# Kernel tuning notes

Measured on AMD Instinct MI355X. Metric: run time of the kernel, lower is better.

Reference implementation:

```python
import jax, jax.numpy as jnp
from jax import lax
import numpy as np

# Bit order convention: pulse index 0 = MSB (sign bit), index 31 = LSB of mantissa.
SHIFTS = jnp.arange(31, -1, -1, dtype=jnp.uint32)  # [32]


def f32_to_pulses(x):
    """float32 [...] -> pulse bits [..., 32] in {0.,1.}"""
    u = lax.bitcast_convert_type(x.astype(jnp.float32), jnp.uint32)
    return ((u[..., None] >> SHIFTS) & jnp.uint32(1)).astype(jnp.float32)


def pulses_to_f32(p):
    """pulse bits [..., 32] -> float32 [...]"""
    bits = (p > 0.5).astype(jnp.uint32)
    u = jnp.sum(bits << SHIFTS, axis=-1).astype(jnp.uint32)
    return lax.bitcast_convert_type(u, jnp.float32)


def setup_inputs() -> dict:
    key = jax.random.key(0)
    kx, kw = jax.random.split(key)
    B, IN, OUT = 256, 1024, 1024
    x_f = jax.random.normal(kx, (B, IN), dtype=jnp.float32)
    w_f = jax.random.normal(kw, (OUT, IN), dtype=jnp.float32) * (1.0 / np.sqrt(IN))
    return {"x": f32_to_pulses(x_f), "weight_pulse": f32_to_pulses(w_f)}


def reference(x, weight_pulse):
    # Decode pulses to IEEE-754 FP32 values (exact: the spiking multiplier/adder
    # implement bit-exact FP32 arithmetic).
    xf = pulses_to_f32(x)              # [B, in]
    wf = pulses_to_f32(weight_pulse)   # [out, in]
    prods = xf[..., None, :] * wf      # [B, out, in]
    # SequentialAccumulator: strictly left-to-right FP32 accumulation (bit-exact
    # deterministic order), expressed as a scan over the in_features axis.
    acc0 = jnp.zeros(prods.shape[:-1], dtype=jnp.float32)  # [B, out]
    acc, _ = lax.scan(lambda a, p: (a + p, None), acc0, jnp.moveaxis(prods, -1, 0))
    # Re-encode the FP32 result to output pulses [B, out, 32].
    return f32_to_pulses(acc)
```

## Files before the change

### kernel.cpp

```cpp
#include <hip/hip_runtime.h>
#include <cstdint>

#define BATCH 256
#define INF   1024
#define OUTF  1024

__device__ __forceinline__ uint32_t assemble_bits(const float4* __restrict__ p4) {
    uint32_t u = 0;
#pragma unroll
    for (int j = 0; j < 8; ++j) {
        float4 v = p4[j];
        int sh = 31 - j * 4;
        u |= (v.x > 0.5f ? 1u : 0u) << sh;
        u |= (v.y > 0.5f ? 1u : 0u) << (sh - 1);
        u |= (v.z > 0.5f ? 1u : 0u) << (sh - 2);
        u |= (v.w > 0.5f ? 1u : 0u) << (sh - 3);
    }
    return u;
}

__global__ __launch_bounds__(256) void decode_pulses(
    const float* __restrict__ pulses, float* __restrict__ out, int n) {
    int i = blockIdx.x * blockDim.x + threadIdx.x;
    if (i >= n) return;
    const float4* p4 = reinterpret_cast<const float4*>(pulses) + (size_t)i * 8;
    out[i] = __uint_as_float(assemble_bits(p4));
}

__global__ __launch_bounds__(256) void gemm_encode(
    const float* __restrict__ xf,
    const float* __restrict__ wf,
    float* __restrict__ out)
{
#pragma clang fp contract(off)
    __shared__ float w_s[64 * 64];
    __shared__ float x_s[8][64];
    const int tx = threadIdx.x, ty = threadIdx.y;
    const int t  = ty * 64 + tx;
    const int o0 = blockIdx.x * 64;
    const int b0 = blockIdx.y * 8;

    const int o_loc = t & 63;
    const int seg0  = t >> 6;
    const float* __restrict__ wbase = wf + (size_t)(o0 + o_loc) * INF;
    const int xr = t >> 4, xs = t & 15;

    float4 wreg[4];
    float4 xreg;

#pragma unroll
    for (int h = 0; h < 4; ++h)
        wreg[h] = *reinterpret_cast<const float4*>(wbase + (seg0 + 4 * h) * 4);
    if (t < 128)
        xreg = *reinterpret_cast<const float4*>(xf + (size_t)(b0 + xr) * INF + xs * 4);
#pragma unroll
    for (int h = 0; h < 4; ++h) {
        const int s = seg0 + 4 * h;
        w_s[(s * 4 + 0) * 64 + o_loc] = wreg[h].x;
        w_s[(s * 4 + 1) * 64 + o_loc] = wreg[h].y;
        w_s[(s * 4 + 2) * 64 + o_loc] = wreg[h].z;
        w_s[(s * 4 + 3) * 64 + o_loc] = wreg[h].w;
    }
    if (t < 128)
        *reinterpret_cast<float4*>(&x_s[xr][xs * 4]) = xreg;
    __syncthreads();

    float acc0 = 0.0f, acc1 = 0.0f;

    for (int kt = 0; kt < 16; ++kt) {
        if (kt < 15) {
            const int k0 = (kt + 1) * 64;
#pragma unroll
            for (int h = 0; h < 4; ++h)
                wreg[h] = *reinterpret_cast<const float4*>(wbase + k0 + (seg0 + 4 * h) * 4);
            if (t < 128)
                xreg = *reinterpret_cast<const float4*>(xf + (size_t)(b0 + xr) * INF + k0 + xs * 4);
        }

        const float* wcol  = w_s + tx;
        const float* xrow0 = x_s[ty * 2];
        const float* xrow1 = x_s[ty * 2 + 1];
#pragma unroll
        for (int k4 = 0; k4 < 16; ++k4) {
            float4 xa = *reinterpret_cast<const float4*>(xrow0 + k4 * 4);
            float4 xb = *reinterpret_cast<const float4*>(xrow1 + k4 * 4);
            float w0 = wcol[(k4 * 4 + 0) * 64];
            float w1 = wcol[(k4 * 4 + 1) * 64];
            float w2 = wcol[(k4 * 4 + 2) * 64];
            float w3 = wcol[(k4 * 4 + 3) * 64];
            acc0 = acc0 + xa.x * w0;
            acc0 = acc0 + xa.y * w1;
            acc0 = acc0 + xa.z * w2;
            acc0 = acc0 + xa.w * w3;
            acc1 = acc1 + xb.x * w0;
            acc1 = acc1 + xb.y * w1;
            acc1 = acc1 + xb.z * w2;
            acc1 = acc1 + xb.w * w3;
        }
        __syncthreads();

        if (kt < 15) {
#pragma unroll
            for (int h = 0; h < 4; ++h) {
                const int s = seg0 + 4 * h;
                w_s[(s * 4 + 0) * 64 + o_loc] = wreg[h].x;
                w_s[(s * 4 + 1) * 64 + o_loc] = wreg[h].y;
                w_s[(s * 4 + 2) * 64 + o_loc] = wreg[h].z;
                w_s[(s * 4 + 3) * 64 + o_loc] = wreg[h].w;
            }
            if (t < 128)
                *reinterpret_cast<float4*>(&x_s[xr][xs * 4]) = xreg;
            __syncthreads();
        }
    }

    const int o = o0 + tx;
    float accs[2] = {acc0, acc1};
#pragma unroll
    for (int q = 0; q < 2; ++q) {
        uint32_t u = __float_as_uint(accs[q]);
        float4* dst = reinterpret_cast<float4*>(out)
                      + ((size_t)(b0 + ty * 2 + q) * OUTF + o) * 8;
#pragma unroll
        for (int j = 0; j < 8; ++j) {
            int sh = 31 - j * 4;
            dst[j] = make_float4((float)((u >> sh) & 1u),
                                 (float)((u >> (sh - 1)) & 1u),
                                 (float)((u >> (sh - 2)) & 1u),
                                 (float)((u >> (sh - 3)) & 1u));
        }
    }
}

extern "C" void kernel_launch(void* const* d_in, const int* in_sizes, int n_in,
                              void* d_out, int out_size, void* d_ws, size_t ws_size,
                              hipStream_t stream) {
    const float* x_pulses = (const float*)d_in[0];
    const float* w_pulses = (const float*)d_in[1];
    float* out = (float*)d_out;

    float* xf = (float*)d_ws;
    float* wf = xf + (size_t)BATCH * INF;

    {
        int n = BATCH * INF;
        decode_pulses<<<(n + 255) / 256, 256, 0, stream>>>(x_pulses, xf, n);
    }
    {
        int n = OUTF * INF;
        decode_pulses<<<n / 256, 256, 0, stream>>>(w_pulses, wf, n);
    }
    {
        dim3 grid(OUTF / 64, BATCH / 8);
        dim3 block(64, 4);
        gemm_encode<<<grid, block, 0, stream>>>(xf, wf, out);
    }
}
```

Before: 251.7 us.

## Store weight tile row-major with XOR swizzle and read x directly from global

The weight tile in shared memory moves from a transposed scalar layout to a per-output-row layout written and read as float4, with an XOR swizzle on 16-byte groups to avoid bank conflicts. Each thread then loads four consecutive k weights in one LDS instruction instead of four scalar reads. The x shared-memory tile is removed, and x rows are read directly from global memory, where they are uniform across a wavefront and should be served by cache. This cuts LDS instruction count but adds global load latency inside the inner loop, without explicit prefetch for x.

```diff
diff --git a/kernel.cpp b/kernel.cpp
--- a/kernel.cpp
+++ b/kernel.cpp
@@ -34,82 +34,67 @@
 {
 #pragma clang fp contract(off)
     __shared__ float w_s[64 * 64];
-    __shared__ float x_s[8][64];
     const int tx = threadIdx.x, ty = threadIdx.y;
     const int t  = ty * 64 + tx;
     const int o0 = blockIdx.x * 64;
     const int b0 = blockIdx.y * 8;
 
     const int o_loc = t & 63;
-    const int seg0  = t >> 6;
+    const int g0    = (t >> 6) * 4;
+    const int swz   = o_loc & 15;
     const float* __restrict__ wbase = wf + (size_t)(o0 + o_loc) * INF;
-    const int xr = t >> 4, xs = t & 15;
+
+    const float* __restrict__ xra = xf + (size_t)(b0 + 2 * ty) * INF;
+    const float* __restrict__ xrb = xra + INF;
 
     float4 wreg[4];
-    float4 xreg;
 
 #pragma unroll
     for (int h = 0; h < 4; ++h)
-        wreg[h] = *reinterpret_cast<const float4*>(wbase + (seg0 + 4 * h) * 4);
-    if (t < 128)
-        xreg = *reinterpret_cast<const float4*>(xf + (size_t)(b0 + xr) * INF + xs * 4);
+        wreg[h] = *reinterpret_cast<const float4*>(wbase + (g0 + h) * 4);
 #pragma unroll
     for (int h = 0; h < 4; ++h) {
-        const int s = seg0 + 4 * h;
-        w_s[(s * 4 + 0) * 64 + o_loc] = wreg[h].x;
-        w_s[(s * 4 + 1) * 64 + o_loc] = wreg[h].y;
-        w_s[(s * 4 + 2) * 64 + o_loc] = wreg[h].z;
-        w_s[(s * 4 + 3) * 64 + o_loc] = wreg[h].w;
+        const int gs = (g0 + h) ^ swz;
+        *reinterpret_cast<float4*>(&w_s[o_loc * 64 + gs * 4]) = wreg[h];
     }
-    if (t < 128)
-        *reinterpret_cast<float4*>(&x_s[xr][xs * 4]) = xreg;
     __syncthreads();
 
     float acc0 = 0.0f, acc1 = 0.0f;
+    const int rswz = tx & 15;
 
     for (int kt = 0; kt < 16; ++kt) {
         if (kt < 15) {
             const int k0 = (kt + 1) * 64;
 #pragma unroll
             for (int h = 0; h < 4; ++h)
-                wreg[h] = *reinterpret_cast<const float4*>(wbase + k0 + (seg0 + 4 * h) * 4);
-            if (t < 128)
-                xreg = *reinterpret_cast<const float4*>(xf + (size_t)(b0 + xr) * INF + k0 + xs * 4);
+                wreg[h] = *reinterpret_cast<const float4*>(wbase + k0 + (g0 + h) * 4);
         }
 
-        const float* wcol  = w_s + tx;
-        const float* xrow0 = x_s[ty * 2];
-        const float* xrow1 = x_s[ty * 2 + 1];
+        const float* xpa = xra + kt * 64;
+        const float* xpb = xrb + kt * 64;
 #pragma unroll
         for (int k4 = 0; k4 < 16; ++k4) {
-            float4 xa = *reinterpret_cast<const float4*>(xrow0 + k4 * 4);
-            float4 xb = *reinterpret_cast<const float4*>(xrow1 + k4 * 4);
-            float w0 = wcol[(k4 * 4 + 0) * 64];
-            float w1 = wcol[(k4 * 4 + 1) * 64];
-            float w2 = wcol[(k4 * 4 + 2) * 64];
-            float w3 = wcol[(k4 * 4 + 3) * 64];
-            acc0 = acc0 + xa.x * w0;
-            acc0 = acc0 + xa.y * w1;
-            acc0 = acc0 + xa.z * w2;
-            acc0 = acc0 + xa.w * w3;
-            acc1 = acc1 + xb.x * w0;
-            acc1 = acc1 + xb.y * w1;
-            acc1 = acc1 + xb.z * w2;
-            acc1 = acc1 + xb.w * w3;
+            float4 w = *reinterpret_cast<const float4*>(
+                &w_s[tx * 64 + ((k4 ^ rswz) * 4)]);
+            float4 a = *reinterpret_cast<const float4*>(xpa + k4 * 4);
+            float4 b = *reinterpret_cast<const float4*>(xpb + k4 * 4);
+            acc0 = acc0 + a.x * w.x;
+            acc0 = acc0 + a.y * w.y;
+            acc0 = acc0 + a.z * w.z;
+            acc0 = acc0 + a.w * w.w;
+            acc1 = acc1 + b.x * w.x;
+            acc1 = acc1 + b.y * w.y;
+            acc1 = acc1 + b.z * w.z;
+            acc1 = acc1 + b.w * w.w;
         }
         __syncthreads();
 
         if (kt < 15) {
 #pragma unroll
             for (int h = 0; h < 4; ++h) {
-                const int s = seg0 + 4 * h;
-                w_s[(s * 4 + 0) * 64 + o_loc] = wreg[h].x;
-                w_s[(s * 4 + 1) * 64 + o_loc] = wreg[h].y;
-                w_s[(s * 4 + 2) * 64 + o_loc] = wreg[h].z;
-                w_s[(s * 4 + 3) * 64 + o_loc] = wreg[h].w;
+                const int gs = (g0 + h) ^ swz;
+                *reinterpret_cast<float4*>(&w_s[o_loc * 64 + gs * 4]) = wreg[h];
             }
-            if (t < 128)
-                *reinterpret_cast<float4*>(&x_s[xr][xs * 4]) = xreg;
             __syncthreads();
         }
     }
```

Result: slower. 301.7 us (+19.9%).
